# Performance work log

Measured on AMD Instinct MI355X. Metric: run time of the kernel, lower is better.

## Reference

```python
import jax, jax.numpy as jnp
import numpy as np

EPS_NORM = 1e-12   # torch F.normalize eps
EPS_SQ = 1e-12     # floor on squared distance before sqrt


def _l2_normalize(x):
    # matches torch F.normalize(x, p=2, dim=1, eps=1e-12)
    n = jnp.sqrt(jnp.sum(x * x, axis=-1, keepdims=True))
    return x / jnp.maximum(n, EPS_NORM)


def setup_inputs() -> dict:
    key = jax.random.key(0)
    k1, k2, k3 = jax.random.split(key, 3)
    N, D, C = 16384, 2048, 8192
    features = jax.random.normal(k1, (N, D), dtype=jnp.float32)
    # prototypes initialized N(0, 10) as in the module
    prototypes = jax.random.normal(k2, (C, D), dtype=jnp.float32) * 10.0
    distance_scale = jnp.ones((1,), dtype=jnp.float32)
    return {"features": features, "prototypes": prototypes, "distance_scale": distance_scale}


def reference(features, prototypes, distance_scale):
    # Both operands are L2-normalized, so ||f - p||^2 = 2 - 2 <f, p>.
    f = _l2_normalize(features)      # [N, D]
    p = _l2_normalize(prototypes)    # [C, D]
    sim = jnp.einsum('nd,cd->nc', f, p)                 # [N, C]
    sq = jnp.maximum(2.0 - 2.0 * sim, EPS_SQ)
    distances = jnp.abs(distance_scale[0]) * jnp.sqrt(sq)
    return -distances
```

## Files before the change

kernel.cpp:

```cpp
#include <hip/hip_runtime.h>
#include <stdint.h>


#define K_DIM 2048
#define BM 256
#define BN 256
#define BK 64
#define NT (K_DIM / BK)

typedef short bf16x8 __attribute__((ext_vector_type(8)));
typedef float f32x4 __attribute__((ext_vector_type(4)));

__device__ __forceinline__ unsigned short f32_to_bf16(float f) {
  unsigned u = __float_as_uint(f);
  unsigned r = 0x7FFFu + ((u >> 16) & 1u);
  return (unsigned short)((u + r) >> 16);
}

__global__ __launch_bounds__(256) void norm_rows_kernel(
    const float* __restrict__ in, unsigned short* __restrict__ out) {
  const int row = blockIdx.x;
  const int t = threadIdx.x;
  const float4* rp = (const float4*)(in + (size_t)row * K_DIM);
  float4 a = rp[t];
  float4 b = rp[t + 256];
  float ss = a.x * a.x + a.y * a.y + a.z * a.z + a.w * a.w +
             b.x * b.x + b.y * b.y + b.z * b.z + b.w * b.w;
#pragma unroll
  for (int off = 32; off > 0; off >>= 1) ss += __shfl_down(ss, off, 64);
  __shared__ float sred[4];
  if ((t & 63) == 0) sred[t >> 6] = ss;
  __syncthreads();
  float tot = sred[0] + sred[1] + sred[2] + sred[3];
  float inv = 1.0f / fmaxf(sqrtf(tot), 1e-12f);
  ushort4 oa, ob;
  oa.x = f32_to_bf16(a.x * inv);
  oa.y = f32_to_bf16(a.y * inv);
  oa.z = f32_to_bf16(a.z * inv);
  oa.w = f32_to_bf16(a.w * inv);
  ob.x = f32_to_bf16(b.x * inv);
  ob.y = f32_to_bf16(b.y * inv);
  ob.z = f32_to_bf16(b.z * inv);
  ob.w = f32_to_bf16(b.w * inv);
  ushort4* op = (ushort4*)(out + (size_t)row * K_DIM);
  op[t] = oa;
  op[t + 256] = ob;
}

__device__ __forceinline__ void async_load16(const void* gptr, uint32_t lds_off,
                                             void* lds_base) {
  typedef __attribute__((address_space(3))) uint32_t lds_u32_t;
  typedef const __attribute__((address_space(1))) uint32_t glb_u32_t;
  glb_u32_t* g = reinterpret_cast<glb_u32_t*>(reinterpret_cast<uintptr_t>(gptr));
  lds_u32_t* l = reinterpret_cast<lds_u32_t*>(
      (uint32_t)(reinterpret_cast<uintptr_t>(lds_base) + lds_off));
  __builtin_amdgcn_global_load_lds(g, l, 16, 0, 0);
}

__device__ __forceinline__ void stage_a(const unsigned short* gA,
                                        unsigned short* lds_, int wave, int buf,
                                        int half, int tt) {
  const unsigned short* s = gA + (size_t)(half * 128) * K_DIM + (size_t)tt * BK;
  uint32_t d = (uint32_t)(buf * 65536 + half * 16384 + wave * 1024);
  async_load16(s, d, lds_);
  async_load16(s + (size_t)64 * K_DIM, d + 8192u, lds_);
}
__device__ __forceinline__ void stage_b(const unsigned short* gB,
                                        unsigned short* lds_, int wave, int buf,
                                        int half, int tt) {
  const unsigned short* s = gB + (size_t)(half * 128) * K_DIM + (size_t)tt * BK;
  uint32_t d = (uint32_t)(buf * 65536 + 32768 + half * 16384 + wave * 1024);
  async_load16(s, d, lds_);
  async_load16(s + (size_t)64 * K_DIM, d + 8192u, lds_);
}

__device__ __forceinline__ void ld_a(bf16x8 (&dst)[4][2],
                                     const unsigned short* lds_, int bufe,
                                     int mh, int wm, int frow, int lxe) {
#pragma unroll
  for (int fi = 0; fi < 4; ++fi)
#pragma unroll
    for (int ks = 0; ks < 2; ++ks)
      dst[fi][ks] = *(const bf16x8*)(lds_ + bufe +
                                     (wm * 128 + mh * 64 + fi * 16 + frow) * 64 +
                                     (lxe ^ (ks << 5)));
}
__device__ __forceinline__ void ld_b(bf16x8 (&dst)[2][2],
                                     const unsigned short* lds_, int bufe,
                                     int nh, int wn, int frow, int lxe) {
#pragma unroll
  for (int fj = 0; fj < 2; ++fj)
#pragma unroll
    for (int ks = 0; ks < 2; ++ks)
      dst[fj][ks] = *(const bf16x8*)(lds_ + bufe + 16384 +
                                     (wn * 64 + nh * 32 + fj * 16 + frow) * 64 +
                                     (lxe ^ (ks << 5)));
}

__device__ __forceinline__ void mfma_quad(f32x4 (&acc)[8][4],
                                          const bf16x8 (&af)[4][2],
                                          const bf16x8 (&bf)[2][2], int mh,
                                          int nh) {
#pragma unroll
  for (int fi = 0; fi < 4; ++fi)
#pragma unroll
    for (int fj = 0; fj < 2; ++fj) {
      f32x4 c = acc[mh * 4 + fi][nh * 2 + fj];
      c = __builtin_amdgcn_mfma_f32_16x16x32_bf16(af[fi][0], bf[fj][0], c, 0, 0, 0);
      c = __builtin_amdgcn_mfma_f32_16x16x32_bf16(af[fi][1], bf[fj][1], c, 0, 0, 0);
      acc[mh * 4 + fi][nh * 2 + fj] = c;
    }
}

#define KTILE(BUF, OBUF, T)                                                   \
  do {                                                                        \
    const int _stb1 = ((T) + 1 < NT) ? (T) + 1 : NT - 1;                      \
    const int _st2 = ((T) + 2 < NT) ? (T) + 2 : NT - 1;                       \
                                                                 \
    ld_a(a0, lds, (BUF)*32768, 0, wm, frow, lxe);                             \
    ld_b(b0, lds, (BUF)*32768, 0, wn, frow, lxe);                             \
    stage_b(gB, lds, wave, OBUF, 1, _stb1);                                   \
    __builtin_amdgcn_s_barrier();                                             \
    asm volatile("s_waitcnt lgkmcnt(0)" ::: "memory");                        \
    __builtin_amdgcn_s_setprio(1);                                            \
    mfma_quad(acc, a0, b0, 0, 0);                                             \
    __builtin_amdgcn_s_setprio(0);                                            \
    __builtin_amdgcn_s_barrier();                                             \
                                                                 \
    ld_a(a1, lds, (BUF)*32768, 1, wm, frow, lxe);                             \
    stage_a(gA, lds, wave, BUF, 0, _st2);                                     \
    __builtin_amdgcn_s_barrier();                                             \
    asm volatile("s_waitcnt lgkmcnt(0)" ::: "memory");                        \
    __builtin_amdgcn_s_setprio(1);                                            \
    mfma_quad(acc, a1, b0, 1, 0);                                             \
    __builtin_amdgcn_s_setprio(0);                                            \
    __builtin_amdgcn_s_barrier();                                             \
                                                                 \
    ld_b(b1, lds, (BUF)*32768, 1, wn, frow, lxe);                             \
    stage_a(gA, lds, wave, BUF, 1, _st2);                                     \
    __builtin_amdgcn_s_barrier();                                             \
    asm volatile("s_waitcnt lgkmcnt(0)" ::: "memory");                        \
    __builtin_amdgcn_s_setprio(1);                                            \
    mfma_quad(acc, a1, b1, 1, 1);                                             \
    __builtin_amdgcn_s_setprio(0);                                            \
    __builtin_amdgcn_s_barrier();                                             \
                                                                 \
    stage_b(gB, lds, wave, BUF, 0, _st2);                                     \
    asm volatile("s_waitcnt vmcnt(6)" ::: "memory");                          \
    __builtin_amdgcn_s_barrier();                                             \
    __builtin_amdgcn_s_setprio(1);                                            \
    mfma_quad(acc, a0, b1, 0, 1);                                             \
    __builtin_amdgcn_s_setprio(0);                                            \
    __builtin_amdgcn_s_barrier();                                             \
  } while (0)

__global__ __launch_bounds__(512, 2) void gemm_bt_dist(
    const unsigned short* __restrict__ A, const unsigned short* __restrict__ B,
    float* __restrict__ Out, const float* __restrict__ scale_ptr, int N,
    int C) {
  __shared__ __align__(16) unsigned short lds[65536];

  const int tid = threadIdx.x;
  const int wave = tid >> 6;
  const int lane = tid & 63;
  const int wm = wave >> 2;
  const int wn = wave & 3;

  const int nwg = gridDim.x;
  const int orig = blockIdx.x;
  const int swz = (orig & 7) * (nwg >> 3) + (orig >> 3);
  const int tiles_n = C / BN;
  const int tm = swz / tiles_n;
  const int tn = swz % tiles_n;
  const int m0 = tm * BM;
  const int n0 = tn * BN;

  const int srow = tid >> 3;
  const int swslot = (tid & 7) ^ (srow & 7);
  const unsigned short* gA = A + (size_t)(m0 + srow) * K_DIM + swslot * 8;
  const unsigned short* gB = B + (size_t)(n0 + srow) * K_DIM + swslot * 8;

  const int frow = lane & 15;
  const int lxe = (((lane >> 4) ^ (lane & 7)) << 3);

  f32x4 acc[8][4] = {};
  bf16x8 a0[4][2], a1[4][2], b0[2][2], b1[2][2];

  stage_a(gA, lds, wave, 0, 0, 0);
  stage_a(gA, lds, wave, 0, 1, 0);
  stage_b(gB, lds, wave, 0, 0, 0);
  stage_b(gB, lds, wave, 0, 1, 0);
  stage_a(gA, lds, wave, 1, 0, 1);
  stage_a(gA, lds, wave, 1, 1, 1);
  stage_b(gB, lds, wave, 1, 0, 1);
  asm volatile("s_waitcnt vmcnt(6)" ::: "memory");
  __builtin_amdgcn_s_barrier();

#pragma unroll 1
  for (int t = 0; t < NT; t += 2) {
    KTILE(0, 1, t);
    KTILE(1, 0, t + 1);
  }

  asm volatile("s_waitcnt vmcnt(0)" ::: "memory");

  const float s = fabsf(scale_ptr[0]);
  const int ocol0 = n0 + wn * 64 + (lane & 15);
  const int orow0 = m0 + wm * 128 + ((lane >> 4) << 2);
#pragma unroll
  for (int ai = 0; ai < 8; ++ai) {
#pragma unroll
    for (int bj = 0; bj < 4; ++bj) {
      f32x4 v = acc[ai][bj];
#pragma unroll
      for (int r = 0; r < 4; ++r) {
        float sq = fmaxf(2.0f - 2.0f * v[r], 1e-12f);
        Out[(size_t)(orow0 + ai * 16 + r) * C + (ocol0 + bj * 16)] =
            -s * sqrtf(sq);
      }
    }
  }
}

extern "C" void kernel_launch(void* const* d_in, const int* in_sizes, int n_in,
                              void* d_out, int out_size, void* d_ws,
                              size_t ws_size, hipStream_t stream) {
  const float* feats = (const float*)d_in[0];
  const float* protos = (const float*)d_in[1];
  const float* dscale = (const float*)d_in[2];
  float* out = (float*)d_out;

  const int N = in_sizes[0] / K_DIM;
  const int C = in_sizes[1] / K_DIM;

  unsigned short* fb = (unsigned short*)d_ws;
  unsigned short* pb = fb + (size_t)N * K_DIM;

  norm_rows_kernel<<<N, 256, 0, stream>>>(feats, fb);
  norm_rows_kernel<<<C, 256, 0, stream>>>(protos, pb);

  const int nwg = (N / BM) * (C / BN);
  gemm_bt_dist<<<dim3(nwg), 512, 0, stream>>>(fb, pb, out, dscale, N, C);
}
```

Baseline: 1.099 ms.

## Use wave-per-row normalization and 8x8 XCD-aware tile grouping in GEMM

The row-normalization kernel now gives each 64-lane wave a whole row, reducing it with xor shuffles and looping grid-stride over rows. This removes the LDS reduction and __syncthreads, and launches a fixed 2048 blocks instead of one block per row. The GEMM block-to-tile mapping is changed so that, for the 2048-tile, 32-column case, each of the 8 XCD-interleaved groups works on 8x8 super-tiles. This is meant to improve L2 reuse of A and B panels within each XCD. The new mapping is hardcoded to this shape, and other shapes fall back to the old swizzle.

After: 1.076 ms. -2.2%, faster.

```diff
diff --git a/kernel.cpp b/kernel.cpp
--- a/kernel.cpp
+++ b/kernel.cpp
@@ -17,34 +17,36 @@
   return (unsigned short)((u + r) >> 16);
 }
 
-__global__ __launch_bounds__(256) void norm_rows_kernel(
-    const float* __restrict__ in, unsigned short* __restrict__ out) {
-  const int row = blockIdx.x;
-  const int t = threadIdx.x;
-  const float4* rp = (const float4*)(in + (size_t)row * K_DIM);
-  float4 a = rp[t];
-  float4 b = rp[t + 256];
-  float ss = a.x * a.x + a.y * a.y + a.z * a.z + a.w * a.w +
-             b.x * b.x + b.y * b.y + b.z * b.z + b.w * b.w;
-#pragma unroll
-  for (int off = 32; off > 0; off >>= 1) ss += __shfl_down(ss, off, 64);
-  __shared__ float sred[4];
-  if ((t & 63) == 0) sred[t >> 6] = ss;
-  __syncthreads();
-  float tot = sred[0] + sred[1] + sred[2] + sred[3];
-  float inv = 1.0f / fmaxf(sqrtf(tot), 1e-12f);
-  ushort4 oa, ob;
-  oa.x = f32_to_bf16(a.x * inv);
-  oa.y = f32_to_bf16(a.y * inv);
-  oa.z = f32_to_bf16(a.z * inv);
-  oa.w = f32_to_bf16(a.w * inv);
-  ob.x = f32_to_bf16(b.x * inv);
-  ob.y = f32_to_bf16(b.y * inv);
-  ob.z = f32_to_bf16(b.z * inv);
-  ob.w = f32_to_bf16(b.w * inv);
-  ushort4* op = (ushort4*)(out + (size_t)row * K_DIM);
-  op[t] = oa;
-  op[t + 256] = ob;
+__global__ __launch_bounds__(256) void norm_rows_wave(
+    const float* __restrict__ in, unsigned short* __restrict__ out,
+    int nrows) {
+  const int lane = threadIdx.x & 63;
+  const int wid = (blockIdx.x << 2) + (threadIdx.x >> 6);
+  const int nw = gridDim.x << 2;
+  for (int row = wid; row < nrows; row += nw) {
+    const float4* rp = (const float4*)(in + (size_t)row * K_DIM);
+    float4 v[8];
+#pragma unroll
+    for (int j = 0; j < 8; ++j) v[j] = rp[lane + (j << 6)];
+    float ss = 0.0f;
+#pragma unroll
+    for (int j = 0; j < 8; ++j)
+      ss += v[j].x * v[j].x + v[j].y * v[j].y + v[j].z * v[j].z +
+            v[j].w * v[j].w;
+#pragma unroll
+    for (int off = 32; off > 0; off >>= 1) ss += __shfl_xor(ss, off, 64);
+    const float inv = 1.0f / fmaxf(sqrtf(ss), 1e-12f);
+    ushort4* op = (ushort4*)(out + (size_t)row * K_DIM);
+#pragma unroll
+    for (int j = 0; j < 8; ++j) {
+      ushort4 o;
+      o.x = f32_to_bf16(v[j].x * inv);
+      o.y = f32_to_bf16(v[j].y * inv);
+      o.z = f32_to_bf16(v[j].z * inv);
+      o.w = f32_to_bf16(v[j].w * inv);
+      op[lane + (j << 6)] = o;
+    }
+  }
 }
 
 __device__ __forceinline__ void async_load16(const void* gptr, uint32_t lds_off,
@@ -168,10 +170,18 @@
 
   const int nwg = gridDim.x;
   const int orig = blockIdx.x;
-  const int swz = (orig & 7) * (nwg >> 3) + (orig >> 3);
   const int tiles_n = C / BN;
-  const int tm = swz / tiles_n;
-  const int tn = swz % tiles_n;
+  int tm, tn;
+  if (nwg == 2048 && tiles_n == 32) {
+    const int x = orig & 7;
+    const int l = orig >> 3;
+    tm = (x << 3) + ((l & 63) >> 3);
+    tn = ((l >> 6) << 3) + (l & 7);
+  } else {
+    const int swz = (orig & 7) * (nwg >> 3) + (orig >> 3);
+    tm = swz / tiles_n;
+    tn = swz % tiles_n;
+  }
   const int m0 = tm * BM;
   const int n0 = tn * BN;
 
@@ -236,8 +246,8 @@
   unsigned short* fb = (unsigned short*)d_ws;
   unsigned short* pb = fb + (size_t)N * K_DIM;
 
-  norm_rows_kernel<<<N, 256, 0, stream>>>(feats, fb);
-  norm_rows_kernel<<<C, 256, 0, stream>>>(protos, pb);
+  norm_rows_wave<<<2048, 256, 0, stream>>>(feats, fb, N);
+  norm_rows_wave<<<2048, 256, 0, stream>>>(protos, pb, C);
 
   const int nwg = (N / BM) * (C / BN);
   gemm_bt_dist<<<dim3(nwg), 512, 0, stream>>>(fb, pb, out, dscale, N, C);
```
